# Kernel tuning notes

Hardware: AMD Instinct MI355X
Metric: run time of the kernel (lower is better)

## Reference

```python
import jax, jax.numpy as jnp
import numpy as np

C = 256          # in_channels == out_channels
L = 131072       # sequence length (multiple of BL)
BL = 64          # dilation == sliding-attention block length
CQ = C // 2      # q/k channels (r1=2)
CV = C // 2      # v channels (r2=2)
ALPHA = 1.0
EPS_IN = 1e-5    # InstanceNorm eps


def setup_inputs() -> dict:
    key = jax.random.key(0)
    ks = jax.random.split(key, 16)
    s = 0.05
    return {
        "x": jax.random.normal(ks[0], (1, C, L), jnp.float32),
        "f": jax.random.normal(ks[1], (1, C, L), jnp.float32),
        "mask": jnp.ones((1, 1, L), jnp.float32),
        # ConvFeedForward: Conv1d(C, C, 3, padding=BL, dilation=BL)
        "Wff": jax.random.normal(ks[2], (C, C, 3), jnp.float32) * s,
        "bff": jax.random.normal(ks[3], (C,), jnp.float32) * s,
        # AttLayer 1x1 convs
        "Wq": jax.random.normal(ks[4], (CQ, C), jnp.float32) * s,
        "bq": jax.random.normal(ks[5], (CQ,), jnp.float32) * s,
        "Wk": jax.random.normal(ks[6], (CQ, C), jnp.float32) * s,
        "bk": jax.random.normal(ks[7], (CQ,), jnp.float32) * s,
        "Wv": jax.random.normal(ks[8], (CV, C), jnp.float32) * s,
        "bv": jax.random.normal(ks[9], (CV,), jnp.float32) * s,
        "Wo": jax.random.normal(ks[10], (C, CV), jnp.float32) * s,
        "bo": jax.random.normal(ks[11], (C,), jnp.float32) * s,
        # AttModule.conv_1x1
        "Wc": jax.random.normal(ks[12], (C, C), jnp.float32) * s,
        "bc": jax.random.normal(ks[13], (C,), jnp.float32) * s,
    }


def _conv1x1(W, b, x):  # x: (B, Cin, L)
    return jnp.einsum('oc,bcl->bol', W, x) + b[None, :, None]


def _forward(x, f, mask, Wff, bff, Wq, bq, Wk, bk, Wv, bv, Wo, bo, Wc, bc):
    # --- ConvFeedForward: dilated conv + ReLU (same-length output) ---
    out = jax.lax.conv_general_dilated(
        x, Wff, window_strides=(1,), padding=[(BL, BL)], rhs_dilation=(BL,),
        dimension_numbers=('NCH', 'OIH', 'NCH')) + bff[None, :, None]
    out = jax.nn.relu(out)  # (1, C, L)

    # --- InstanceNorm1d (affine=False, biased var) ---
    mu = out.mean(axis=-1, keepdims=True)
    var = out.var(axis=-1, keepdims=True)
    xn = (out - mu) * jax.lax.rsqrt(var + EPS_IN)

    # --- AttLayer (sliding_att, decoder: value from f) ---
    q = _conv1x1(Wq, bq, xn)   # (1, CQ, L)
    k = _conv1x1(Wk, bk, xn)   # (1, CQ, L)
    v = _conv1x1(Wv, bv, f)    # (1, CV, L)

    nb = L // BL
    half = BL // 2
    pm = mask[:, 0:1, :]                         # (1,1,L) padding mask
    # pad halo of BL//2 zeros on each side of k, v, padding_mask
    kp = jnp.pad(k, ((0, 0), (0, 0), (half, half)))
    vp = jnp.pad(v, ((0, 0), (0, 0), (half, half)))
    mp = jnp.pad(pm, ((0, 0), (0, 0), (half, half)))
    # window index: block i sees [i*BL, i*BL + 2*BL) of the padded sequence
    idx = jnp.arange(nb)[:, None] * BL + jnp.arange(2 * BL)[None, :]  # (nb, 2BL)
    kw = kp[:, :, idx]   # (1, CQ, nb, 2BL)
    vw = vp[:, :, idx]   # (1, CV, nb, 2BL)
    mw = mp[:, 0, idx]   # (1, nb, 2BL)

    # window mask: query i attends keys [i, i+BL) within the 2BL window
    d = jnp.arange(2 * BL)[None, :] - jnp.arange(BL)[:, None]
    wm = ((d >= 0) & (d < BL)).astype(x.dtype)          # (BL, 2BL)
    fm = wm[None, None] * mw[:, :, None, :]             # (1, nb, BL, 2BL)

    qb = q.reshape(1, CQ, nb, BL)
    energy = jnp.einsum('bcnl,bcnm->bnlm', qb, kw) / np.sqrt(CQ).astype(x.dtype)
    att = jax.nn.softmax(energy + jnp.log(fm + 1e-6), axis=-1) * fm
    ov = jnp.einsum('bcnm,bnlm->bcnl', vw, att)         # (1, CV, nb, BL)
    oo = jnp.einsum('oc,bcnl->bonl', Wo, jax.nn.relu(ov)) + bo[None, :, None, None]
    att_out = oo.reshape(1, C, L) * pm                  # (1, C, L)

    # --- scaled residual + 1x1 conv + (dropout=identity) + masked residual ---
    h = ALPHA * att_out + out
    h = _conv1x1(Wc, bc, h)
    return (x + h) * mask


def reference(x, f, mask, Wff, bff, Wq, bq, Wk, bk, Wv, bv, Wo, bo, Wc, bc):
    return _forward(x, f, mask, Wff, bff, Wq, bq, Wk, bk, Wv, bv, Wo, bo, Wc, bc)
```

## Files before the change

kernel.cpp:

```cpp
#include <hip/hip_runtime.h>

#define L_LEN 131072
#define NB    2048
#define NT    1024

typedef unsigned short u16;
typedef __attribute__((ext_vector_type(4))) float f32x4;
typedef __attribute__((ext_vector_type(8))) short s16x8;
typedef __attribute__((ext_vector_type(4))) short s16x4;

#define WS_OUTT  0ull
#define WS_QT    67108864ull
#define WS_PSUM  100663296ull
#define WS_PSQ   101711872ull
#define WS_MEAN  102760448ull
#define WS_RSTD  102761472ull
#define WS_WFFB  102762496ull
#define WS_WQKB  103155712ull
#define WS_WVB   103286784ull
#define WS_WOB   103352320ull
#define WS_WCB   103417856ull
#define WS_BQKP  103548928ull

__device__ __forceinline__ u16 f2bf(float v){
  union { float f; unsigned u; } a; a.f = v;
  unsigned r = a.u + 0x7fffu + ((a.u >> 16) & 1u);
  return (u16)(r >> 16);
}
__device__ __forceinline__ float bf2f(u16 u){
  union { unsigned u; float f; } a; a.u = ((unsigned)u) << 16; return a.f;
}
__device__ __forceinline__ unsigned cvtpk(float a, float b){
  unsigned r;
  asm("v_cvt_pk_bf16_f32 %0, %1, %2" : "=v"(r) : "v"(a), "v"(b));
  return r;
}
__device__ __forceinline__ f32x4 mfma16(s16x8 a, s16x8 b, f32x4 c){
  return __builtin_amdgcn_mfma_f32_16x16x32_bf16(a, b, c, 0, 0, 0);
}
__device__ __forceinline__ s16x8 ld8(const void* p){ return *(const s16x8*)p; }
__device__ __forceinline__ void gl_lds16(const void* g, void* l){
  __builtin_amdgcn_global_load_lds(
      (const __attribute__((address_space(1))) unsigned int*)g,
      (__attribute__((address_space(3))) unsigned int*)l, 16, 0, 0);
}

__global__ __launch_bounds__(256) void k_prep(
    const float* __restrict__ Wff, const float* __restrict__ Wv,
    const float* __restrict__ Wo,  const float* __restrict__ Wc,
    short* __restrict__ wffb, short* __restrict__ wvb,
    short* __restrict__ wob,  short* __restrict__ wcb)
{
  int i = blockIdx.x * 256 + threadIdx.x;
  if (i < 196608){
    int o = i / 768, kk = i % 768;
    int t = kk >> 8, c = kk & 255;
    wffb[i] = (short)f2bf(Wff[(o*256 + c)*3 + t]);
  } else if (i < 229376){ int j = i - 196608; wvb[j] = (short)f2bf(Wv[j]); }
  else if (i < 262144){ int j = i - 229376; wob[j] = (short)f2bf(Wo[j]); }
  else if (i < 327680){ int j = i - 262144; wcb[j] = (short)f2bf(Wc[j]); }
}

__global__ __launch_bounds__(512, 4) void k_conv(
    const float* __restrict__ x, const short* __restrict__ wffb,
    const float* __restrict__ bff, u16* __restrict__ outT,
    float* __restrict__ psum, float* __restrict__ psq)
{
  __shared__ u16 wlds[2*8192];
  const int bid = blockIdx.x;
  const int wg = (bid & 7) * 128 + (bid >> 3);
  const int l0 = wg * 128;
  const int tid = threadIdx.x;
  const int w = tid >> 6, lane = tid & 63, p = lane & 15, g = lane >> 4;

  auto stage = [&](int it, int buf){
    const int t = it >> 3, kk = it & 7;
    const int kbase = t*256 + kk*32;
    #pragma unroll
    for (int j = 0; j < 2; ++j){
      const int och = 32*w + 16*j + (lane >> 2);
      const int srcblk = (lane & 3) ^ ((lane >> 3) & 3);
      const short* src = wffb + (size_t)och*768 + kbase + srcblk*8;
      u16* dst = &wlds[buf*8192 + (32*w + 16*j)*32];
      gl_lds16(src, dst);
    }
  };
  auto loadx = [&](int it, float* r){
    const int t = it >> 3, kk = it & 7;
    const int pa = l0 + 16*w + p + 64*t - 64;
    const int pac = min(max(pa, 0), L_LEN - 1);
    const bool ok = (pa >= 0) && (pa < L_LEN);
    #pragma unroll
    for (int j = 0; j < 8; ++j){
      const int c = kk*32 + 8*g + j;
      float v = x[(size_t)c*L_LEN + pac];
      r[j] = ok ? v : 0.f;
    }
  };
  auto pack8 = [&](const float* r) -> s16x8 {
    union { unsigned u[4]; s16x8 v; } t;
    t.u[0] = cvtpk(r[0], r[1]); t.u[1] = cvtpk(r[2], r[3]);
    t.u[2] = cvtpk(r[4], r[5]); t.u[3] = cvtpk(r[6], r[7]);
    return t.v;
  };

  float r[8];
  loadx(0, r);
  stage(0, 0);
  __syncthreads();
  s16x8 a_cur = pack8(r), a_nxt;

  f32x4 acc[16] = {};
  const int rb = p*32 + ((g ^ ((p >> 1) & 3)) * 8);
  #pragma unroll 1
  for (int it = 0; it < 24; ++it){
    const int cur = it & 1;
    if (it < 23){ stage(it + 1, cur ^ 1); loadx(it + 1, r); }
    #pragma unroll
    for (int fn = 0; fn < 16; ++fn){
      s16x8 bw = ld8(&wlds[cur*8192 + rb + fn*512]);
      acc[fn] = mfma16(bw, a_cur, acc[fn]);
    }
    if (it < 23) a_nxt = pack8(r);
    __syncthreads();
    a_cur = a_nxt;
  }

  float* sred = (float*)wlds;
  const int pos = l0 + 16*w + p;
  #pragma unroll
  for (int fn = 0; fn < 16; ++fn){
    const int och0 = 16*fn + 4*g;
    s16x4 pk;
    float sv[4], qv[4];
    #pragma unroll
    for (int i = 0; i < 4; ++i){
      float val = fmaxf(acc[fn][i] + bff[och0 + i], 0.f);
      pk[i] = (short)f2bf(val);
      sv[i] = val; qv[i] = val*val;
    }
    *(s16x4*)(outT + (size_t)pos*256 + och0) = pk;
    #pragma unroll
    for (int i = 0; i < 4; ++i){
      #pragma unroll
      for (int d = 1; d < 16; d <<= 1){
        sv[i] += __shfl_xor(sv[i], d, 16);
        qv[i] += __shfl_xor(qv[i], d, 16);
      }
      if (p == 0){
        sred[(w*256 + och0 + i)*2 + 0] = sv[i];
        sred[(w*256 + och0 + i)*2 + 1] = qv[i];
      }
    }
  }
  __syncthreads();
  if (tid < 256){
    float a = 0.f, b = 0.f;
    #pragma unroll
    for (int ww = 0; ww < 8; ++ww){
      a += sred[(ww*256 + tid)*2 + 0];
      b += sred[(ww*256 + tid)*2 + 1];
    }
    psum[(size_t)tid*NT + wg] = a;
    psq [(size_t)tid*NT + wg] = b;
  }
}

__global__ __launch_bounds__(256) void k_stats(
    const float* __restrict__ psum, const float* __restrict__ psq,
    float* __restrict__ mean, float* __restrict__ rstd)
{
  __shared__ float ss[256], sq[256];
  const int ch = blockIdx.x, tid = threadIdx.x;
  float a = 0.f, b = 0.f;
  for (int j = tid; j < NT; j += 256){ a += psum[(size_t)ch*NT + j]; b += psq[(size_t)ch*NT + j]; }
  ss[tid] = a; sq[tid] = b;
  __syncthreads();
  for (int st = 128; st > 0; st >>= 1){
    if (tid < st){ ss[tid] += ss[tid+st]; sq[tid] += sq[tid+st]; }
    __syncthreads();
  }
  if (tid == 0){
    float m = ss[0] / (float)L_LEN;
    float v = sq[0] / (float)L_LEN - m*m;
    mean[ch] = m;
    rstd[ch] = rsqrtf(v + 1e-5f);
  }
}

__global__ __launch_bounds__(256) void k_adj(
    const float* __restrict__ Wq, const float* __restrict__ Wk,
    const float* __restrict__ bq, const float* __restrict__ bk,
    const float* __restrict__ mean, const float* __restrict__ rstd,
    short* __restrict__ wqkb, float* __restrict__ bqkp)
{
  __shared__ float red[256];
  const int o = blockIdx.x, c = threadIdx.x;
  const float* src = (o < 128) ? (Wq + (size_t)o*256) : (Wk + (size_t)(o-128)*256);
  const float bias = (o < 128) ? bq[o] : bk[o-128];
  float wv = src[c] * rstd[c];
  wqkb[o*256 + c] = (short)f2bf(wv);
  red[c] = wv * mean[c];
  __syncthreads();
  for (int st = 128; st > 0; st >>= 1){
    if (c < st) red[c] += red[c+st];
    __syncthreads();
  }
  if (c == 0) bqkp[o] = bias - red[0];
}

__global__ __launch_bounds__(512, 4) void k_v(
    const float* __restrict__ fin, const short* __restrict__ wvb,
    const float* __restrict__ bv, u16* __restrict__ vout)
{
  __shared__ u16 xs[2*128*40];
  const int wg = blockIdx.x, l0 = wg * 128;
  const int tid = threadIdx.x;
  const int w = tid >> 6, lane = tid & 63, p = lane & 15, g = lane >> 4;
  const int cl = tid >> 4, posq = tid & 15;

  {
    #pragma unroll
    for (int u = 0; u < 2; ++u){
      const int row = 8*posq + 4*u;
      f32x4 v = *(const f32x4*)(fin + (size_t)cl*L_LEN + l0 + row);
      const unsigned r01 = cvtpk(v[0], v[1]);
      const unsigned r23 = cvtpk(v[2], v[3]);
      xs[(row+0)*40 + (cl ^ (8*(((row+0)>>2)&3)))] = (u16)(r01 & 0xffffu);
      xs[(row+1)*40 + (cl ^ (8*(((row+1)>>2)&3)))] = (u16)(r01 >> 16);
      xs[(row+2)*40 + (cl ^ (8*(((row+2)>>2)&3)))] = (u16)(r23 & 0xffffu);
      xs[(row+3)*40 + (cl ^ (8*(((row+3)>>2)&3)))] = (u16)(r23 >> 16);
    }
  }
  __syncthreads();

  f32x4 acc[8] = {};
  #pragma unroll 1
  for (int cg = 0; cg < 8; ++cg){
    const int cur = (cg & 1) * 5120;
    const int nxt = ((cg + 1) & 1) * 5120;
    f32x4 vv[2];
    const bool have = (cg < 7);
    if (have){
      #pragma unroll
      for (int u = 0; u < 2; ++u){
        const int row = 8*posq + 4*u;
        vv[u] = *(const f32x4*)(fin + (size_t)((cg+1)*32 + cl)*L_LEN + l0 + row);
      }
    }
    s16x8 af = ld8(wvb + (size_t)(16*w + p)*256 + cg*32 + 8*g);
    #pragma unroll
    for (int fn = 0; fn < 8; ++fn){
      const int row = 16*fn + p;
      s16x8 b = ld8(&xs[cur + row*40 + ((8*g) ^ (8*((row>>2)&3)))]);
      acc[fn] = mfma16(af, b, acc[fn]);
    }
    if (have){
      #pragma unroll
      for (int u = 0; u < 2; ++u){
        const int row = 8*posq + 4*u;
        const unsigned r01 = cvtpk(vv[u][0], vv[u][1]);
        const unsigned r23 = cvtpk(vv[u][2], vv[u][3]);
        xs[nxt + (row+0)*40 + (cl ^ (8*(((row+0)>>2)&3)))] = (u16)(r01 & 0xffffu);
        xs[nxt + (row+1)*40 + (cl ^ (8*(((row+1)>>2)&3)))] = (u16)(r01 >> 16);
        xs[nxt + (row+2)*40 + (cl ^ (8*(((row+2)>>2)&3)))] = (u16)(r23 & 0xffffu);
        xs[nxt + (row+3)*40 + (cl ^ (8*(((row+3)>>2)&3)))] = (u16)(r23 >> 16);
      }
    }
    __syncthreads();
  }
  #pragma unroll
  for (int fn = 0; fn < 8; ++fn){
    #pragma unroll
    for (int i = 0; i < 4; ++i){
      const int cv = 16*w + 4*g + i;
      vout[(size_t)cv*L_LEN + l0 + 16*fn + p] = f2bf(acc[fn][i] + bv[cv]);
    }
  }
}

__global__ __launch_bounds__(512, 2) void k_qk(
    const u16* __restrict__ outT, const short* __restrict__ wqkb,
    const float* __restrict__ bqkp, u16* __restrict__ qT, u16* __restrict__ kT)
{
  extern __shared__ u16 tile[];
  const int wg = blockIdx.x, l0 = wg * 128;
  const int tid = threadIdx.x;
  const int w = tid >> 6, lane = tid & 63, p = lane & 15, g = lane >> 4;
  #pragma unroll
  for (int rep = 0; rep < 8; ++rep){
    const int idx = rep*512 + tid;
    const int r = idx >> 5, cc = idx & 31;
    s16x8 vput = ld8(outT + (size_t)(l0 + r)*256 + cc*8);
    *(s16x8*)(&tile[r*256 + ((cc*8) ^ ((r&7)<<3))]) = vput;
  }
  __syncthreads();
  f32x4 acc[2][8] = {};
  #pragma unroll
  for (int kk = 0; kk < 8; ++kk){
    s16x8 af[2];
    af[0] = ld8(wqkb + (size_t)(32*w +      p)*256 + 32*kk + 8*g);
    af[1] = ld8(wqkb + (size_t)(32*w + 16 + p)*256 + 32*kk + 8*g);
    #pragma unroll
    for (int fn = 0; fn < 8; ++fn){
      const int r = 16*fn + p;
      s16x8 b = ld8(&tile[r*256 + ((32*kk + 8*g) ^ ((r&7)<<3))]);
      acc[0][fn] = mfma16(af[0], b, acc[0][fn]);
      acc[1][fn] = mfma16(af[1], b, acc[1][fn]);
    }
  }
  #pragma unroll
  for (int fm = 0; fm < 2; ++fm){
    const int R0 = 32*w + 16*fm + 4*g;
    #pragma unroll
    for (int fn = 0; fn < 8; ++fn){
      s16x4 pk;
      #pragma unroll
      for (int i = 0; i < 4; ++i) pk[i] = (short)f2bf(acc[fm][fn][i] + bqkp[R0+i]);
      const size_t row = (size_t)(l0 + 16*fn + p);
      if (R0 < 128) *(s16x4*)(qT + row*128 + R0)       = pk;
      else          *(s16x4*)(kT + row*128 + R0 - 128) = pk;
    }
  }
}

__global__ __launch_bounds__(256, 4) void k_attn(
    const u16* __restrict__ qT, const u16* __restrict__ kT,
    const u16* __restrict__ vg, const short* __restrict__ wob,
    const float* __restrict__ bo, const float* __restrict__ mask,
    u16* __restrict__ outT)
{
  __shared__ u16 klds[16384];
  __shared__ float maskw[128];
  const int tid = threadIdx.x;
  const int w = tid >> 6, lane = tid & 63, p = lane & 15, g = lane >> 4;
  const int n = blockIdx.x, s = n * 64;
  const float SCALE = 0.08838834764831845f;

  #pragma unroll
  for (int rep = 0; rep < 8; ++rep){
    const int idx = rep*256 + tid;
    const int m = idx >> 4, cc = idx & 15;
    const int gpos = s - 32 + m;
    s16x8 vput = {};
    if (gpos >= 0 && gpos < L_LEN) vput = ld8(kT + (size_t)gpos*128 + cc*8);
    *(s16x8*)(&klds[m*128 + ((cc*8) ^ ((m&7)<<3))]) = vput;
  }
  if (tid < 128){
    const int gp = s - 32 + tid;
    maskw[tid] = (gp >= 0 && gp < L_LEN) ? mask[gp] : 0.f;
  }
  __syncthreads();

  f32x4 e[8] = {};
  #pragma unroll
  for (int kk = 0; kk < 4; ++kk){
    s16x8 aq = ld8(qT + (size_t)(s + 16*w + p)*128 + 32*kk + 8*g);
    #pragma unroll
    for (int fn = 0; fn < 8; ++fn){
      const int m = 16*fn + p;
      s16x8 b = ld8(&klds[m*128 + ((32*kk + 8*g) ^ ((m&7)<<3))]);
      e[fn] = mfma16(aq, b, e[fn]);
    }
  }
  float M[4] = {-1e30f,-1e30f,-1e30f,-1e30f};
  float S[4] = {0.f,0.f,0.f,0.f};
  #pragma unroll
  for (int fn = 0; fn < 8; ++fn){
    #pragma unroll
    for (int i = 0; i < 4; ++i){
      const int mm = 16*fn + p;
      const int l_ = 16*w + 4*g + i;
      const int d = mm - l_;
      const float fmv = (d >= 0 && d < 64) ? maskw[mm] : 0.f;
      const float z = e[fn][i]*SCALE + __logf(fmv + 1e-6f);
      e[fn][i] = z;
      M[i] = fmaxf(M[i], z);
    }
  }
  #pragma unroll
  for (int i = 0; i < 4; ++i){
    #pragma unroll
    for (int d = 1; d < 16; d <<= 1) M[i] = fmaxf(M[i], __shfl_xor(M[i], d, 16));
  }
  #pragma unroll
  for (int fn = 0; fn < 8; ++fn){
    #pragma unroll
    for (int i = 0; i < 4; ++i){
      const float pv = __expf(e[fn][i] - M[i]);
      e[fn][i] = pv;
      S[i] += pv;
    }
  }
  #pragma unroll
  for (int i = 0; i < 4; ++i){
    #pragma unroll
    for (int d = 1; d < 16; d <<= 1) S[i] += __shfl_xor(S[i], d, 16);
  }
  float rinv[4];
  #pragma unroll
  for (int i = 0; i < 4; ++i) rinv[i] = 1.f / S[i];
  __syncthreads();
  #pragma unroll
  for (int fn = 0; fn < 8; ++fn){
    #pragma unroll
    for (int i = 0; i < 4; ++i){
      const int mm = 16*fn + p;
      const int l_ = 16*w + 4*g + i;
      const int d = mm - l_;
      const float fmv = (d >= 0 && d < 64) ? maskw[mm] : 0.f;
      klds[l_*128 + (mm ^ ((l_&7)<<3))] = f2bf(e[fn][i] * rinv[i] * fmv);
    }
  }
  __syncthreads();

  f32x4 accp[2][4] = {};
  #pragma unroll
  for (int kk = 0; kk < 4; ++kk){
    int gp0 = s - 32 + 32*kk + 8*g;
    gp0 = max(0, min(gp0, L_LEN - 8));
    s16x8 a0 = ld8(vg + (size_t)(32*w +      p)*L_LEN + gp0);
    s16x8 a1 = ld8(vg + (size_t)(32*w + 16 + p)*L_LEN + gp0);
    #pragma unroll
    for (int fn = 0; fn < 4; ++fn){
      const int l_ = 16*fn + p;
      s16x8 b = ld8(&klds[l_*128 + ((32*kk + 8*g) ^ ((l_&7)<<3))]);
      accp[0][fn] = mfma16(a0, b, accp[0][fn]);
      accp[1][fn] = mfma16(a1, b, accp[1][fn]);
    }
  }
  #pragma unroll
  for (int fm = 0; fm < 2; ++fm){
    #pragma unroll
    for (int fn = 0; fn < 4; ++fn){
      const int l_ = 16*fn + p;
      s16x4 pk;
      #pragma unroll
      for (int i = 0; i < 4; ++i) pk[i] = (short)f2bf(fmaxf(accp[fm][fn][i], 0.f));
      const int cv0 = 32*w + 16*fm + 4*g;
      *(s16x4*)(&klds[8192 + l_*128 + (cv0 ^ ((l_&7)<<3))]) = pk;
    }
  }
  __syncthreads();

  f32x4 acco[4][4] = {};
  #pragma unroll
  for (int kk = 0; kk < 4; ++kk){
    s16x8 a[4];
    #pragma unroll
    for (int fm = 0; fm < 4; ++fm)
      a[fm] = ld8(wob + (size_t)(64*w + 16*fm + p)*128 + 32*kk + 8*g);
    #pragma unroll
    for (int fn = 0; fn < 4; ++fn){
      const int l_ = 16*fn + p;
      s16x8 b = ld8(&klds[8192 + l_*128 + ((32*kk + 8*g) ^ ((l_&7)<<3))]);
      #pragma unroll
      for (int fm = 0; fm < 4; ++fm) acco[fm][fn] = mfma16(a[fm], b, acco[fm][fn]);
    }
  }
  #pragma unroll
  for (int fm = 0; fm < 4; ++fm){
    const int o0 = 64*w + 16*fm + 4*g;
    #pragma unroll
    for (int fn = 0; fn < 4; ++fn){
      const int l_ = 16*fn + p;
      const float pml = maskw[32 + l_];
      u16* hp = outT + (size_t)(s + l_)*256 + o0;
      s16x4 res = *(const s16x4*)hp;
      s16x4 pk;
      #pragma unroll
      for (int i = 0; i < 4; ++i){
        float hv = (acco[fm][fn][i] + bo[o0+i]) * pml + bf2f((u16)res[i]);
        pk[i] = (short)f2bf(hv);
      }
      *(s16x4*)hp = pk;
    }
  }
}

__global__ __launch_bounds__(512, 2) void k_wc(
    const u16* __restrict__ hT, const short* __restrict__ wcb,
    const float* __restrict__ bc, const float* __restrict__ x,
    const float* __restrict__ mask, float* __restrict__ dout)
{
  extern __shared__ u16 tile[];
  const int wg = blockIdx.x, l0 = wg * 128;
  const int tid = threadIdx.x;
  const int w = tid >> 6, lane = tid & 63, p = lane & 15, g = lane >> 4;
  #pragma unroll
  for (int rep = 0; rep < 8; ++rep){
    const int idx = rep*512 + tid;
    const int r = idx >> 5, cc = idx & 31;
    s16x8 vput = ld8(hT + (size_t)(l0 + r)*256 + cc*8);
    *(s16x8*)(&tile[r*256 + ((cc*8) ^ ((r&7)<<3))]) = vput;
  }
  __syncthreads();
  f32x4 acc[2][8] = {};
  #pragma unroll
  for (int kk = 0; kk < 8; ++kk){
    s16x8 af[2];
    af[0] = ld8(wcb + (size_t)(32*w +      p)*256 + 32*kk + 8*g);
    af[1] = ld8(wcb + (size_t)(32*w + 16 + p)*256 + 32*kk + 8*g);
    #pragma unroll
    for (int fn = 0; fn < 8; ++fn){
      const int r = 16*fn + p;
      s16x8 b = ld8(&tile[r*256 + ((32*kk + 8*g) ^ ((r&7)<<3))]);
      acc[0][fn] = mfma16(af[0], b, acc[0][fn]);
      acc[1][fn] = mfma16(af[1], b, acc[1][fn]);
    }
  }
  #pragma unroll
  for (int fm = 0; fm < 2; ++fm){
    const int o0 = 32*w + 16*fm + 4*g;
    #pragma unroll
    for (int fn = 0; fn < 8; ++fn){
      const int pos = l0 + 16*fn + p;
      const float mk = mask[pos];
      #pragma unroll
      for (int i = 0; i < 4; ++i){
        const size_t idx = (size_t)(o0+i)*L_LEN + pos;
        dout[idx] = (x[idx] + acc[fm][fn][i] + bc[o0+i]) * mk;
      }
    }
  }
}

extern "C" void kernel_launch(void* const* d_in, const int* in_sizes, int n_in,
                              void* d_out, int out_size, void* d_ws, size_t ws_size,
                              hipStream_t stream)
{
  (void)in_sizes; (void)n_in; (void)out_size; (void)ws_size;
  const float* x    = (const float*)d_in[0];
  const float* f    = (const float*)d_in[1];
  const float* mask = (const float*)d_in[2];
  const float* Wff  = (const float*)d_in[3];
  const float* bff  = (const float*)d_in[4];
  const float* Wq   = (const float*)d_in[5];
  const float* bq   = (const float*)d_in[6];
  const float* Wk   = (const float*)d_in[7];
  const float* bk   = (const float*)d_in[8];
  const float* Wv   = (const float*)d_in[9];
  const float* bv   = (const float*)d_in[10];
  const float* Wo   = (const float*)d_in[11];
  const float* bo   = (const float*)d_in[12];
  const float* Wc   = (const float*)d_in[13];
  const float* bc   = (const float*)d_in[14];

  char* ws = (char*)d_ws;
  u16*   outT = (u16*)(ws + WS_OUTT);
  u16*   qT   = (u16*)(ws + WS_QT);
  float* psum = (float*)(ws + WS_PSUM);
  float* psq  = (float*)(ws + WS_PSQ);
  float* mean = (float*)(ws + WS_MEAN);
  float* rstd = (float*)(ws + WS_RSTD);
  short* wffb = (short*)(ws + WS_WFFB);
  short* wqkb = (short*)(ws + WS_WQKB);
  short* wvb  = (short*)(ws + WS_WVB);
  short* wob  = (short*)(ws + WS_WOB);
  short* wcb  = (short*)(ws + WS_WCB);
  float* bqkp = (float*)(ws + WS_BQKP);

  u16* vbuf = (u16*)d_out;
  u16* ktb  = (u16*)((char*)d_out + 33554432);

  (void)hipFuncSetAttribute((const void*)k_qk,
                            hipFuncAttributeMaxDynamicSharedMemorySize, 65536);
  (void)hipFuncSetAttribute((const void*)k_wc,
                            hipFuncAttributeMaxDynamicSharedMemorySize, 65536);

  k_prep <<<1280, 256, 0, stream>>>(Wff, Wv, Wo, Wc, wffb, wvb, wob, wcb);
  k_conv <<<NT,   512, 0, stream>>>(x, wffb, bff, outT, psum, psq);
  k_stats<<<256,  256, 0, stream>>>(psum, psq, mean, rstd);
  k_adj  <<<256,  256, 0, stream>>>(Wq, Wk, bq, bk, mean, rstd, wqkb, bqkp);
  k_v    <<<NT,   512, 0, stream>>>(f, wvb, bv, vbuf);
  k_qk   <<<NT,   512, 65536, stream>>>(outT, wqkb, bqkp, qT, ktb);
  k_attn <<<NB,   256, 0, stream>>>(qT, ktb, vbuf, wob, bo, mask, outT);
  k_wc   <<<NT,   512, 65536, stream>>>(outT, wcb, bc, x, mask, (float*)d_out);
}
```

Before: 380.0 us.

## Pre-transpose x to bf16 position-major and restructure dilated conv tiling

Adds a kernel that converts x to bf16 in a position-major layout, stored in spare output space. The dilated conv now stages a shared window of x rows into LDS once per channel group and reuses it across the three taps. Weights are read directly from global memory as the A operand, using a 4x4 MFMA tile per wave. This replaces strided fp32 gathers and in-loop conversion with coalesced async loads, at the cost of an extra pass over x and uncached weight loads inside the loop.

New measurement: 415.2 us. 9.3% more time.

```diff
diff --git a/kernel.cpp b/kernel.cpp
--- a/kernel.cpp
+++ b/kernel.cpp
@@ -21,6 +21,7 @@
 #define WS_WOB   103352320ull
 #define WS_WCB   103417856ull
 #define WS_BQKP  103548928ull
+#define WS_ZP    103549952ull
 
 __device__ __forceinline__ u16 f2bf(float v){
   union { float f; unsigned u; } a; a.f = v;
@@ -49,7 +50,7 @@
     const float* __restrict__ Wff, const float* __restrict__ Wv,
     const float* __restrict__ Wo,  const float* __restrict__ Wc,
     short* __restrict__ wffb, short* __restrict__ wvb,
-    short* __restrict__ wob,  short* __restrict__ wcb)
+    short* __restrict__ wob,  short* __restrict__ wcb, u16* __restrict__ zp)
 {
   int i = blockIdx.x * 256 + threadIdx.x;
   if (i < 196608){
@@ -59,87 +60,107 @@
   } else if (i < 229376){ int j = i - 196608; wvb[j] = (short)f2bf(Wv[j]); }
   else if (i < 262144){ int j = i - 229376; wob[j] = (short)f2bf(Wo[j]); }
   else if (i < 327680){ int j = i - 262144; wcb[j] = (short)f2bf(Wc[j]); }
+  if (blockIdx.x == 0 && threadIdx.x < 32) zp[threadIdx.x] = 0;
+}
+
+__global__ __launch_bounds__(256) void k_xbfT(
+    const float* __restrict__ x, u16* __restrict__ xbfT)
+{
+  __shared__ u16 t[64*264];
+  const int l0 = blockIdx.x * 64, tid = threadIdx.x;
+  const int chb = tid >> 4, pq = tid & 15;
+  #pragma unroll
+  for (int rep = 0; rep < 16; ++rep){
+    const int ch = rep*16 + chb;
+    const int pos0 = pq*4;
+    f32x4 v = *(const f32x4*)(x + (size_t)ch*L_LEN + l0 + pos0);
+    const unsigned u01 = cvtpk(v[0], v[1]), u23 = cvtpk(v[2], v[3]);
+    t[(pos0+0)*264 + ch] = (u16)(u01 & 0xffffu);
+    t[(pos0+1)*264 + ch] = (u16)(u01 >> 16);
+    t[(pos0+2)*264 + ch] = (u16)(u23 & 0xffffu);
+    t[(pos0+3)*264 + ch] = (u16)(u23 >> 16);
+  }
+  __syncthreads();
+  #pragma unroll
+  for (int rep = 0; rep < 8; ++rep){
+    const int idx = rep*256 + tid;
+    const int row = idx >> 5, j = idx & 31;
+    s16x8 vv = ld8(&t[row*264 + 8*j]);
+    *(s16x8*)(xbfT + (size_t)(l0 + row)*256 + 8*j) = vv;
+  }
 }
 
 __global__ __launch_bounds__(512, 4) void k_conv(
-    const float* __restrict__ x, const short* __restrict__ wffb,
-    const float* __restrict__ bff, u16* __restrict__ outT,
+    const float* __restrict__ xunused, const u16* __restrict__ xbfT,
+    const short* __restrict__ wffb, const float* __restrict__ bff,
+    const u16* __restrict__ zp, u16* __restrict__ outT,
     float* __restrict__ psum, float* __restrict__ psq)
 {
-  __shared__ u16 wlds[2*8192];
+  __shared__ u16 wbuf[2*256*32];
   const int bid = blockIdx.x;
   const int wg = (bid & 7) * 128 + (bid >> 3);
   const int l0 = wg * 128;
   const int tid = threadIdx.x;
   const int w = tid >> 6, lane = tid & 63, p = lane & 15, g = lane >> 4;
-
-  auto stage = [&](int it, int buf){
-    const int t = it >> 3, kk = it & 7;
-    const int kbase = t*256 + kk*32;
-    #pragma unroll
-    for (int j = 0; j < 2; ++j){
-      const int och = 32*w + 16*j + (lane >> 2);
-      const int srcblk = (lane & 3) ^ ((lane >> 3) & 3);
-      const short* src = wffb + (size_t)och*768 + kbase + srcblk*8;
-      u16* dst = &wlds[buf*8192 + (32*w + 16*j)*32];
+  const int wo = w >> 1, wp = w & 1;
+
+  auto stage = [&](int cg, int buf){
+    #pragma unroll
+    for (int gi = 0; gi < 2; ++gi){
+      const int rw = 32*w + 16*gi + (lane >> 2);
+      const int slot = lane & 3;
+      const int cb = slot ^ (((rw >> 2) ^ rw) & 3);
+      const int wpos = l0 - 64 + rw;
+      const u16* src = (wpos >= 0 && wpos < L_LEN)
+                     ? (xbfT + (size_t)wpos*256 + cg*32 + cb*8) : zp;
+      u16* dst = &wbuf[buf*8192 + (32*w + 16*gi)*32];
       gl_lds16(src, dst);
     }
   };
-  auto loadx = [&](int it, float* r){
-    const int t = it >> 3, kk = it & 7;
-    const int pa = l0 + 16*w + p + 64*t - 64;
-    const int pac = min(max(pa, 0), L_LEN - 1);
-    const bool ok = (pa >= 0) && (pa < L_LEN);
-    #pragma unroll
-    for (int j = 0; j < 8; ++j){
-      const int c = kk*32 + 8*g + j;
-      float v = x[(size_t)c*L_LEN + pac];
-      r[j] = ok ? v : 0.f;
-    }
-  };
-  auto pack8 = [&](const float* r) -> s16x8 {
-    union { unsigned u[4]; s16x8 v; } t;
-    t.u[0] = cvtpk(r[0], r[1]); t.u[1] = cvtpk(r[2], r[3]);
-    t.u[2] = cvtpk(r[4], r[5]); t.u[3] = cvtpk(r[6], r[7]);
-    return t.v;
-  };
-
-  float r[8];
-  loadx(0, r);
+
   stage(0, 0);
   __syncthreads();
-  s16x8 a_cur = pack8(r), a_nxt;
-
-  f32x4 acc[16] = {};
-  const int rb = p*32 + ((g ^ ((p >> 1) & 3)) * 8);
+
+  f32x4 acc[4][4] = {};
   #pragma unroll 1
-  for (int it = 0; it < 24; ++it){
-    const int cur = it & 1;
-    if (it < 23){ stage(it + 1, cur ^ 1); loadx(it + 1, r); }
-    #pragma unroll
-    for (int fn = 0; fn < 16; ++fn){
-      s16x8 bw = ld8(&wlds[cur*8192 + rb + fn*512]);
-      acc[fn] = mfma16(bw, a_cur, acc[fn]);
-    }
-    if (it < 23) a_nxt = pack8(r);
+  for (int cg = 0; cg < 8; ++cg){
+    const int cur = cg & 1;
+    if (cg < 7) stage(cg + 1, cur ^ 1);
+    #pragma unroll
+    for (int t = 0; t < 3; ++t){
+      s16x8 a[4];
+      #pragma unroll
+      for (int fm = 0; fm < 4; ++fm)
+        a[fm] = ld8(wffb + (size_t)(64*wo + 16*fm + p)*768 + t*256 + cg*32 + 8*g);
+      #pragma unroll
+      for (int fn = 0; fn < 4; ++fn){
+        const int r = 64*t + 64*wp + 16*fn + p;
+        s16x8 b = ld8(&wbuf[cur*8192 + r*32 + ((g ^ (((r >> 2) ^ r) & 3)) * 8)]);
+        #pragma unroll
+        for (int fm = 0; fm < 4; ++fm)
+          acc[fm][fn] = mfma16(a[fm], b, acc[fm][fn]);
+      }
+    }
     __syncthreads();
-    a_cur = a_nxt;
-  }
-
-  float* sred = (float*)wlds;
-  const int pos = l0 + 16*w + p;
-  #pragma unroll
-  for (int fn = 0; fn < 16; ++fn){
-    const int och0 = 16*fn + 4*g;
-    s16x4 pk;
-    float sv[4], qv[4];
-    #pragma unroll
-    for (int i = 0; i < 4; ++i){
-      float val = fmaxf(acc[fn][i] + bff[och0 + i], 0.f);
-      pk[i] = (short)f2bf(val);
-      sv[i] = val; qv[i] = val*val;
-    }
-    *(s16x4*)(outT + (size_t)pos*256 + och0) = pk;
+  }
+
+  float* sf = (float*)wbuf;
+  #pragma unroll
+  for (int fm = 0; fm < 4; ++fm){
+    const int o0 = 64*wo + 16*fm + 4*g;
+    float sv[4] = {0,0,0,0}, qv[4] = {0,0,0,0};
+    #pragma unroll
+    for (int fn = 0; fn < 4; ++fn){
+      const int pos = 64*wp + 16*fn + p;
+      s16x4 pk;
+      #pragma unroll
+      for (int i = 0; i < 4; ++i){
+        float val = fmaxf(acc[fm][fn][i] + bff[o0 + i], 0.f);
+        pk[i] = (short)f2bf(val);
+        sv[i] += val; qv[i] += val*val;
+      }
+      *(s16x4*)(outT + (size_t)(l0 + pos)*256 + o0) = pk;
+    }
     #pragma unroll
     for (int i = 0; i < 4; ++i){
       #pragma unroll
@@ -148,21 +169,15 @@
         qv[i] += __shfl_xor(qv[i], d, 16);
       }
       if (p == 0){
-        sred[(w*256 + och0 + i)*2 + 0] = sv[i];
-        sred[(w*256 + och0 + i)*2 + 1] = qv[i];
+        sf[(wp*256 + o0 + i)*2 + 0] = sv[i];
+        sf[(wp*256 + o0 + i)*2 + 1] = qv[i];
       }
     }
   }
   __syncthreads();
   if (tid < 256){
-    float a = 0.f, b = 0.f;
-    #pragma unroll
-    for (int ww = 0; ww < 8; ++ww){
-      a += sred[(ww*256 + tid)*2 + 0];
-      b += sred[(ww*256 + tid)*2 + 1];
-    }
-    psum[(size_t)tid*NT + wg] = a;
-    psq [(size_t)tid*NT + wg] = b;
+    psum[(size_t)tid*NT + wg] = sf[(0*256 + tid)*2 + 0] + sf[(1*256 + tid)*2 + 0];
+    psq [(size_t)tid*NT + wg] = sf[(0*256 + tid)*2 + 1] + sf[(1*256 + tid)*2 + 1];
   }
 }
 
@@ -559,17 +574,20 @@
   short* wob  = (short*)(ws + WS_WOB);
   short* wcb  = (short*)(ws + WS_WCB);
   float* bqkp = (float*)(ws + WS_BQKP);
+  u16*   zp   = (u16*)(ws + WS_ZP);
 
   u16* vbuf = (u16*)d_out;
   u16* ktb  = (u16*)((char*)d_out + 33554432);
+  u16* xbfT = (u16*)((char*)d_out + 67108864);
 
   (void)hipFuncSetAttribute((const void*)k_qk,
                             hipFuncAttributeMaxDynamicSharedMemorySize, 65536);
   (void)hipFuncSetAttribute((const void*)k_wc,
                             hipFuncAttributeMaxDynamicSharedMemorySize, 65536);
 
-  k_prep <<<1280, 256, 0, stream>>>(Wff, Wv, Wo, Wc, wffb, wvb, wob, wcb);
-  k_conv <<<NT,   512, 0, stream>>>(x, wffb, bff, outT, psum, psq);
+  k_prep <<<1280, 256, 0, stream>>>(Wff, Wv, Wo, Wc, wffb, wvb, wob, wcb, zp);
+  k_xbfT <<<2048, 256, 0, stream>>>(x, xbfT);
+  k_conv <<<NT,   512, 0, stream>>>(x, xbfT, wffb, bff, zp, outT, psum, psq);
   k_stats<<<256,  256, 0, stream>>>(psum, psq, mean, rstd);
   k_adj  <<<256,  256, 0, stream>>>(Wq, Wk, bq, bk, mean, rstd, wqkb, bqkp);
   k_v    <<<NT,   512, 0, stream>>>(f, wvb, bv, vbuf);
```
